# Performance work log

Hardware: AMD Instinct MI355X
Metric: run time of the kernel (lower is better)

Reference implementation:

```python
import jax, jax.numpy as jnp
import numpy as np

DIM = 1024
N_HEADS = 16
HEAD_DIM = DIM // N_HEADS
SCALE = HEAD_DIM ** -0.5


def setup_inputs() -> dict:
    key = jax.random.key(0)
    ks = jax.random.split(key, 5)
    x = jax.random.normal(ks[0], (4, 2048, DIM), dtype=jnp.float32)
    # nn.Linear weights stored as [out, in]; we keep [in, out] for x @ W
    w_qkv = jax.random.normal(ks[1], (DIM, 3 * DIM), dtype=jnp.float32) * (DIM ** -0.5)
    b_qkv = jnp.zeros((3 * DIM,), dtype=jnp.float32)
    w_proj = jax.random.normal(ks[2], (DIM, DIM), dtype=jnp.float32) * (DIM ** -0.5)
    b_proj = jnp.zeros((DIM,), dtype=jnp.float32)
    return {"x": x, "w_qkv": w_qkv, "b_qkv": b_qkv, "w_proj": w_proj, "b_proj": b_proj}


def reference(x, w_qkv, b_qkv, w_proj, b_proj):
    B, S, D = x.shape
    qkv = x @ w_qkv + b_qkv                                   # [B,S,3D]
    qkv = qkv.reshape(B, S, 3, N_HEADS, HEAD_DIM)
    qkv = jnp.transpose(qkv, (2, 0, 3, 1, 4))                 # [3,B,H,S,hd]
    q, k, v = qkv[0], qkv[1], qkv[2]
    attn = jnp.einsum("bhqd,bhkd->bhqk", q, k) * SCALE        # [B,H,S,S]
    attn = jax.nn.softmax(attn, axis=-1)
    out = jnp.einsum("bhqk,bhkd->bhqd", attn, v)              # [B,H,S,hd]
    out = jnp.transpose(out, (0, 2, 1, 3)).reshape(B, S, D)   # [B,S,D]
    return out @ w_proj + b_proj
```

## Files before the change

kernel.cpp:

```cpp
#include <hip/hip_runtime.h>
#include <hip/hip_bf16.h>

typedef float f32x4 __attribute__((ext_vector_type(4)));
typedef short bf16x8 __attribute__((ext_vector_type(8)));
typedef unsigned short ushort8 __attribute__((ext_vector_type(8)));

__device__ __forceinline__ unsigned short f2bf(float f) {
    union { float f; unsigned u; } v; v.f = f;
    unsigned r = v.u + 0x7fffu + ((v.u >> 16) & 1u);
    return (unsigned short)(r >> 16);
}

__device__ __forceinline__ unsigned short f2bf_hw(float f) {
    union { __hip_bfloat16 b; unsigned short u; } cv;
    cv.b = __float2bfloat16(f);
    return cv.u;
}

#define GLDS16(g, l)                                                        \
    __builtin_amdgcn_global_load_lds(                                       \
        (const __attribute__((address_space(1))) unsigned int*)(const void*)(g), \
        (__attribute__((address_space(3))) unsigned int*)(void*)(l), 16, 0, 0)

__global__ __launch_bounds__(256) void k_cvt(const float* __restrict__ in,
                                             unsigned short* __restrict__ out, int n8) {
    int i = blockIdx.x * 256 + threadIdx.x;
    if (i >= n8) return;
    float4 a = ((const float4*)in)[i * 2];
    float4 b = ((const float4*)in)[i * 2 + 1];
    ushort8 o = { f2bf(a.x), f2bf(a.y), f2bf(a.z), f2bf(a.w),
                  f2bf(b.x), f2bf(b.y), f2bf(b.z), f2bf(b.w) };
    ((ushort8*)out)[i] = o;
}

__global__ __launch_bounds__(256) void k_tpose(const float* __restrict__ in,
                                               unsigned short* __restrict__ out,
                                               int R, int C) {
    __shared__ float t[32][33];
    int c0 = blockIdx.x * 32, r0 = blockIdx.y * 32;
    int tx = threadIdx.x, ty = threadIdx.y;
#pragma unroll
    for (int i = 0; i < 4; i++)
        t[ty + i * 8][tx] = in[(size_t)(r0 + ty + i * 8) * C + c0 + tx];
    __syncthreads();
#pragma unroll
    for (int i = 0; i < 4; i++)
        out[(size_t)(c0 + ty + i * 8) * R + r0 + tx] = f2bf(t[tx][ty + i * 8]);
}

template <int MODE>
__global__ __launch_bounds__(256)
void k_gemm(const unsigned short* __restrict__ A, const unsigned short* __restrict__ Bt,
            const float* __restrict__ bias, int M, int N, int K,
            float* __restrict__ outF, unsigned short* __restrict__ q_ws,
            unsigned short* __restrict__ k_ws, unsigned short* __restrict__ vt_ws) {
    __shared__ __attribute__((aligned(16))) unsigned short Ash[128 * 32];
    __shared__ __attribute__((aligned(16))) unsigned short Bsh[128 * 32];
    __shared__ __attribute__((aligned(16))) unsigned short Vt[(MODE == 1) ? 128 * 136 : 8];
    int tid = threadIdx.x;
    int lane = tid & 63, w = tid >> 6;
    int wr = w >> 1, wc = w & 1;

    int nbx = gridDim.x;
    int flat = blockIdx.y * nbx + blockIdx.x;
    int cpx = (nbx * gridDim.y) >> 3;
    int wg = (flat & 7) * cpx + (flat >> 3);
    int m0 = (wg / nbx) * 128, n0 = (wg % nbx) * 128;

    f32x4 acc[4][4] = {};

    int srow = tid >> 2, sk = (tid & 3) * 8;
    const unsigned short* aS0 = A + (size_t)(m0 + srow) * K + sk;
    const unsigned short* aS1 = A + (size_t)(m0 + 64 + srow) * K + sk;
    const unsigned short* bS0 = Bt + (size_t)(n0 + srow) * K + sk;
    const unsigned short* bS1 = Bt + (size_t)(n0 + 64 + srow) * K + sk;
    unsigned short* aD0 = Ash + w * 512;
    unsigned short* aD1 = Ash + 2048 + w * 512;
    unsigned short* bD0 = Bsh + w * 512;
    unsigned short* bD1 = Bsh + 2048 + w * 512;

    int ko = (lane >> 4) * 8;
    int arow = (wr * 64 + (lane & 15)) * 32;
    int brow = (wc * 64 + (lane & 15)) * 32;

    for (int k0 = 0; k0 < K; k0 += 32) {
        GLDS16(aS0, aD0);
        GLDS16(aS1, aD1);
        GLDS16(bS0, bD0);
        GLDS16(bS1, bD1);
        aS0 += 32; aS1 += 32; bS0 += 32; bS1 += 32;
        __syncthreads();
        bf16x8 af[4], bfr[4];
#pragma unroll
        for (int i = 0; i < 4; i++) {
            af[i]  = *(const bf16x8*)&Ash[arow + i * 16 * 32 + ko];
            bfr[i] = *(const bf16x8*)&Bsh[brow + i * 16 * 32 + ko];
        }
#pragma unroll
        for (int i = 0; i < 4; i++)
#pragma unroll
            for (int j = 0; j < 4; j++)
                acc[i][j] = __builtin_amdgcn_mfma_f32_16x16x32_bf16(af[i], bfr[j], acc[i][j], 0, 0, 0);
        __syncthreads();
    }

    int colBase = n0 + wc * 64 + (lane & 15);
    int rowBase = m0 + wr * 64 + ((lane >> 4) << 2);

    if constexpr (MODE == 1) {
        if (n0 >= 2048) {
#pragma unroll
            for (int i = 0; i < 4; i++)
#pragma unroll
                for (int j = 0; j < 4; j++)
#pragma unroll
                    for (int r = 0; r < 4; r++) {
                        int nl = wc * 64 + j * 16 + (lane & 15);
                        int ml = wr * 64 + i * 16 + ((lane >> 4) << 2) + r;
                        Vt[nl * 136 + ml] = f2bf(acc[i][j][r] + bias[n0 + nl]);
                    }
            __syncthreads();
            int row = tid >> 1, col0 = (tid & 1) * 64;
            int rem = (n0 + row) & 1023;
            unsigned short* dst = vt_ws
                + ((size_t)((m0 >> 11) * 16 + (rem >> 6)) * 64 + (rem & 63)) * 2048
                + (m0 & 2047) + col0;
            const unsigned short* src = &Vt[row * 136 + col0];
#pragma unroll
            for (int q2 = 0; q2 < 8; q2++)
                ((uint4*)dst)[q2] = ((const uint4*)src)[q2];
            return;
        }
    }

#pragma unroll
    for (int i = 0; i < 4; i++)
#pragma unroll
        for (int j = 0; j < 4; j++)
#pragma unroll
            for (int r = 0; r < 4; r++) {
                int m = rowBase + i * 16 + r;
                int n = colBase + j * 16;
                float v = acc[i][j][r] + bias[n];
                if constexpr (MODE == 0) {
                    outF[(size_t)m * N + n] = v;
                } else {
                    int which = n >> 10, rem = n & 1023;
                    int h = rem >> 6, d = rem & 63;
                    int b = m >> 11, s = m & 2047;
                    int bh = b * 16 + h;
                    if (which == 0)
                        q_ws[((size_t)bh * 2048 + s) * 64 + d] = f2bf(v * 0.125f);
                    else
                        k_ws[((size_t)bh * 2048 + s) * 64 + d] = f2bf(v);
                }
            }
}

__global__ __launch_bounds__(256)
void k_attn(const unsigned short* __restrict__ q_ws, const unsigned short* __restrict__ k_ws,
            const unsigned short* __restrict__ vt_ws, unsigned short* __restrict__ o_ws) {
    __shared__ __attribute__((aligned(16))) unsigned short Ksh[2][64 * 64];
    __shared__ __attribute__((aligned(16))) unsigned short Vsh[2][64 * 64];
    __shared__ __attribute__((aligned(16))) unsigned short Psh[128 * 72];
    int tid = threadIdx.x, lane = tid & 63, w = tid >> 6;
    int l15 = lane & 15, g = lane >> 4;

    int flat = blockIdx.y * 16 + blockIdx.x;
    int wg = (flat & 7) * 128 + (flat >> 3);
    int bh = wg >> 4;
    int q0 = (wg & 15) * 128;
    int b = bh >> 4, h = bh & 15;

    const unsigned short* qp = q_ws + (size_t)bh * 2048 * 64;
    const unsigned short* kp = k_ws + (size_t)bh * 2048 * 64;
    const unsigned short* vp = vt_ws + (size_t)bh * 64 * 2048;

    int ko = g * 8;
    bf16x8 qf[2][2];
#pragma unroll
    for (int half = 0; half < 2; half++) {
        const unsigned short* qr = qp + (size_t)(q0 + w * 32 + half * 16 + l15) * 64;
        qf[half][0] = *(const bf16x8*)(qr + ko);
        qf[half][1] = *(const bf16x8*)(qr + 32 + ko);
    }

    f32x4 oacc[2][4] = {};
    float lacc[2][4] = {};

    int srow = tid >> 2, squad = tid & 3;
    int ssw = (srow & 7) << 3;
    int sbase = srow * 64;
    int sc0 = (squad * 16) ^ ssw;
    int sc1 = (squad * 16 + 8) ^ ssw;

    const unsigned short* kNext = kp + (size_t)srow * 64 + squad * 16;
    const unsigned short* vNext = vp + (size_t)srow * 2048 + squad * 16;

    uint4 kr0, kr1, vr0, vr1;
#define LOADT()                                                                \
    {                                                                          \
        kr0 = *(const uint4*)kNext; kr1 = *(const uint4*)(kNext + 8);          \
        vr0 = *(const uint4*)vNext; vr1 = *(const uint4*)(vNext + 8);          \
        kNext += 64 * 64; vNext += 64;                                         \
    }
#define STORET(BUF)                                                            \
    {                                                                          \
        *(uint4*)&Ksh[BUF][sbase + sc0] = kr0;                                 \
        *(uint4*)&Ksh[BUF][sbase + sc1] = kr1;                                 \
        *(uint4*)&Vsh[BUF][sbase + sc0] = vr0;                                 \
        *(uint4*)&Vsh[BUF][sbase + sc1] = vr1;                                 \
    }

    LOADT();
    STORET(0);
    __syncthreads();

    for (int t = 0; t < 32; t++) {
        int cur = t & 1;
        if (t < 31) LOADT();

        f32x4 s[2][4];
        __builtin_amdgcn_s_setprio(1);
#pragma unroll
        for (int ct = 0; ct < 4; ct++) {
            int krow = ct * 16 + l15;
            int ksw = (krow & 7) << 3;
            const unsigned short* kb = &Ksh[cur][krow * 64];
            bf16x8 kb0 = *(const bf16x8*)&kb[ko ^ ksw];
            bf16x8 kb1 = *(const bf16x8*)&kb[(32 + ko) ^ ksw];
#pragma unroll
            for (int half = 0; half < 2; half++) {
                f32x4 sa = {};
                sa = __builtin_amdgcn_mfma_f32_16x16x32_bf16(qf[half][0], kb0, sa, 0, 0, 0);
                sa = __builtin_amdgcn_mfma_f32_16x16x32_bf16(qf[half][1], kb1, sa, 0, 0, 0);
                s[half][ct] = sa;
            }
        }
        __builtin_amdgcn_s_setprio(0);

#pragma unroll
        for (int half = 0; half < 2; half++)
#pragma unroll
            for (int r = 0; r < 4; r++) {
                int prow = (w * 32 + half * 16 + 4 * g + r) * 72;
#pragma unroll
                for (int ct = 0; ct < 4; ct++) {
                    float p = __expf(s[half][ct][r]);
                    lacc[half][r] += p;
                    Psh[prow + ct * 16 + l15] = f2bf_hw(p);
                }
            }

        __syncthreads();

        bf16x8 pa[2][2];
#pragma unroll
        for (int half = 0; half < 2; half++) {
            int parow = (w * 32 + half * 16 + l15) * 72;
            pa[half][0] = *(const bf16x8*)&Psh[parow + ko];
            pa[half][1] = *(const bf16x8*)&Psh[parow + 32 + ko];
        }
        __builtin_amdgcn_s_setprio(1);
#pragma unroll
        for (int ct = 0; ct < 4; ct++) {
            int vrow = ct * 16 + l15;
            int vsw = (vrow & 7) << 3;
            const unsigned short* vb = &Vsh[cur][vrow * 64];
            bf16x8 vb0 = *(const bf16x8*)&vb[ko ^ vsw];
            bf16x8 vb1 = *(const bf16x8*)&vb[(32 + ko) ^ vsw];
#pragma unroll
            for (int half = 0; half < 2; half++) {
                oacc[half][ct] = __builtin_amdgcn_mfma_f32_16x16x32_bf16(pa[half][0], vb0, oacc[half][ct], 0, 0, 0);
                oacc[half][ct] = __builtin_amdgcn_mfma_f32_16x16x32_bf16(pa[half][1], vb1, oacc[half][ct], 0, 0, 0);
            }
        }
        __builtin_amdgcn_s_setprio(0);

        if (t < 31) STORET(cur ^ 1);
        __syncthreads();
    }
#undef LOADT
#undef STORET

#pragma unroll
    for (int half = 0; half < 2; half++)
#pragma unroll
        for (int r = 0; r < 4; r++) {
            float lf = lacc[half][r];
#pragma unroll
            for (int off = 8; off; off >>= 1) lf += __shfl_xor(lf, off);
            float inv = 1.0f / lf;
            int srw = q0 + w * 32 + half * 16 + 4 * g + r;
#pragma unroll
            for (int ct = 0; ct < 4; ct++) {
                int d = ct * 16 + l15;
                o_ws[((size_t)(b * 2048 + srw) * 16 + h) * 64 + d] = f2bf_hw(oacc[half][ct][r] * inv);
            }
        }
}

extern "C" void kernel_launch(void* const* d_in, const int* in_sizes, int n_in,
                              void* d_out, int out_size, void* d_ws, size_t ws_size,
                              hipStream_t stream) {
    const float* x      = (const float*)d_in[0];
    const float* w_qkv  = (const float*)d_in[1];
    const float* b_qkv  = (const float*)d_in[2];
    const float* w_proj = (const float*)d_in[3];
    const float* b_proj = (const float*)d_in[4];
    float* out = (float*)d_out;

    char* ws = (char*)d_ws;
    unsigned short* xb  = (unsigned short*)(ws);
    unsigned short* wqt = (unsigned short*)(ws + 16777216);
    unsigned short* wpt = (unsigned short*)(ws + 23068672);
    unsigned short* qw  = (unsigned short*)(ws + 25165824);
    unsigned short* kw  = (unsigned short*)(ws + 41943040);
    unsigned short* vtw = (unsigned short*)(ws + 58720256);
    unsigned short* ow  = (unsigned short*)(ws + 75497472);

    k_cvt<<<4096, 256, 0, stream>>>(x, xb, 1048576);
    k_tpose<<<dim3(96, 32), dim3(32, 8), 0, stream>>>(w_qkv, wqt, 1024, 3072);
    k_tpose<<<dim3(32, 32), dim3(32, 8), 0, stream>>>(w_proj, wpt, 1024, 1024);
    k_gemm<1><<<dim3(24, 64), 256, 0, stream>>>(xb, wqt, b_qkv, 8192, 3072, 1024,
                                                nullptr, qw, kw, vtw);
    k_attn<<<dim3(16, 64), 256, 0, stream>>>(qw, kw, vtw, ow);
    k_gemm<0><<<dim3(8, 64), 256, 0, stream>>>(ow, wpt, b_proj, 8192, 1024, 1024,
                                               out, nullptr, nullptr, nullptr);
}
```

Baseline: 241.9 us.

## Single-buffer attention K/V LDS tiles and alias GEMM shared buffers

The attention kernel drops its double-buffered K/V shared-memory tiles for single buffers. The next tile's global loads are moved to after the QK^T MMAs, and the register-held tile is stored at the top of each iteration before a barrier. The QKV GEMM now aliases its A/B staging buffers with the V-transpose scratch buffer to shrink LDS. Both changes lower LDS per block to allow more resident workgroups, at the cost of an extra barrier and less load/compute overlap per iteration.

```diff
diff --git a/kernel.cpp b/kernel.cpp
--- a/kernel.cpp
+++ b/kernel.cpp
@@ -54,9 +54,10 @@
             const float* __restrict__ bias, int M, int N, int K,
             float* __restrict__ outF, unsigned short* __restrict__ q_ws,
             unsigned short* __restrict__ k_ws, unsigned short* __restrict__ vt_ws) {
-    __shared__ __attribute__((aligned(16))) unsigned short Ash[128 * 32];
-    __shared__ __attribute__((aligned(16))) unsigned short Bsh[128 * 32];
-    __shared__ __attribute__((aligned(16))) unsigned short Vt[(MODE == 1) ? 128 * 136 : 8];
+    __shared__ __attribute__((aligned(16))) unsigned short SMEM[(MODE == 1) ? 128 * 136
+                                                                            : 128 * 64];
+    unsigned short* Ash = SMEM;
+    unsigned short* Bsh = SMEM + 128 * 32;
     int tid = threadIdx.x;
     int lane = tid & 63, w = tid >> 6;
     int wr = w >> 1, wc = w & 1;
@@ -109,6 +110,7 @@
 
     if constexpr (MODE == 1) {
         if (n0 >= 2048) {
+            unsigned short* Vt = SMEM;
 #pragma unroll
             for (int i = 0; i < 4; i++)
 #pragma unroll
@@ -160,8 +162,8 @@
 __global__ __launch_bounds__(256)
 void k_attn(const unsigned short* __restrict__ q_ws, const unsigned short* __restrict__ k_ws,
             const unsigned short* __restrict__ vt_ws, unsigned short* __restrict__ o_ws) {
-    __shared__ __attribute__((aligned(16))) unsigned short Ksh[2][64 * 64];
-    __shared__ __attribute__((aligned(16))) unsigned short Vsh[2][64 * 64];
+    __shared__ __attribute__((aligned(16))) unsigned short Ksh[64 * 64];
+    __shared__ __attribute__((aligned(16))) unsigned short Vsh[64 * 64];
     __shared__ __attribute__((aligned(16))) unsigned short Psh[128 * 72];
     int tid = threadIdx.x, lane = tid & 63, w = tid >> 6;
     int l15 = lane & 15, g = lane >> 4;
@@ -204,21 +206,19 @@
         vr0 = *(const uint4*)vNext; vr1 = *(const uint4*)(vNext + 8);          \
         kNext += 64 * 64; vNext += 64;                                         \
     }
-#define STORET(BUF)                                                            \
+#define STORET()                                                               \
     {                                                                          \
-        *(uint4*)&Ksh[BUF][sbase + sc0] = kr0;                                 \
-        *(uint4*)&Ksh[BUF][sbase + sc1] = kr1;                                 \
-        *(uint4*)&Vsh[BUF][sbase + sc0] = vr0;                                 \
-        *(uint4*)&Vsh[BUF][sbase + sc1] = vr1;                                 \
+        *(uint4*)&Ksh[sbase + sc0] = kr0;                                      \
+        *(uint4*)&Ksh[sbase + sc1] = kr1;                                      \
+        *(uint4*)&Vsh[sbase + sc0] = vr0;                                      \
+        *(uint4*)&Vsh[sbase + sc1] = vr1;                                      \
     }
 
     LOADT();
-    STORET(0);
-    __syncthreads();
 
     for (int t = 0; t < 32; t++) {
-        int cur = t & 1;
-        if (t < 31) LOADT();
+        STORET();
+        __syncthreads();
 
         f32x4 s[2][4];
         __builtin_amdgcn_s_setprio(1);
@@ -226,7 +226,7 @@
         for (int ct = 0; ct < 4; ct++) {
             int krow = ct * 16 + l15;
             int ksw = (krow & 7) << 3;
-            const unsigned short* kb = &Ksh[cur][krow * 64];
+            const unsigned short* kb = &Ksh[krow * 64];
             bf16x8 kb0 = *(const bf16x8*)&kb[ko ^ ksw];
             bf16x8 kb1 = *(const bf16x8*)&kb[(32 + ko) ^ ksw];
 #pragma unroll
@@ -239,6 +239,8 @@
         }
         __builtin_amdgcn_s_setprio(0);
 
+        if (t < 31) LOADT();
+
 #pragma unroll
         for (int half = 0; half < 2; half++)
 #pragma unroll
@@ -266,7 +268,7 @@
         for (int ct = 0; ct < 4; ct++) {
             int vrow = ct * 16 + l15;
             int vsw = (vrow & 7) << 3;
-            const unsigned short* vb = &Vsh[cur][vrow * 64];
+            const unsigned short* vb = &Vsh[vrow * 64];
             bf16x8 vb0 = *(const bf16x8*)&vb[ko ^ vsw];
             bf16x8 vb1 = *(const bf16x8*)&vb[(32 + ko) ^ vsw];
 #pragma unroll
@@ -277,7 +279,6 @@
         }
         __builtin_amdgcn_s_setprio(0);
 
-        if (t < 31) STORET(cur ^ 1);
         __syncthreads();
     }
 #undef LOADT
```

Result: no change. 240.9 us (-0.4%).
